# Optimization experiments

Measured on AMD Instinct MI355X. Metric: run time of the kernel, lower is better.

## Reference

```python
import jax, jax.numpy as jnp
import numpy as np
from jax import lax

T_LEN, BATCH, D_IN, D_HID, N_LAYERS = 512, 32, 512, 512, 4


def setup_inputs() -> dict:
    key = jax.random.key(0)
    kx, kw, ku = jax.random.split(key, 3)
    x = jax.random.normal(kx, (T_LEN, BATCH, D_IN), dtype=jnp.float32)
    # xavier-ish scale on input kernels to keep the relu recurrence stable
    W = jax.random.normal(kw, (N_LAYERS, D_HID, D_IN), dtype=jnp.float32) * (1.0 / np.sqrt(D_IN))
    b = jnp.zeros((N_LAYERS, D_HID), dtype=jnp.float32)
    # diagonal recurrent weights in [0,1) so |u|<=1 (non-exploding)
    u = jax.random.uniform(ku, (N_LAYERS, D_HID), dtype=jnp.float32)
    return {"x": x, "W": W, "b": b, "u": u}


def _indrnn_layer(x, W_l, b_l, u_l):
    # x: [T, B, Din]; precompute input projection as one big GEMM
    xh = jnp.einsum('tbd,hd->tbh', x, W_l) + b_l  # [T, B, Dh]
    h0 = jnp.zeros((x.shape[1], W_l.shape[0]), dtype=x.dtype)

    def step(h, xh_t):
        h_new = jax.nn.relu(xh_t + u_l * h)
        return h_new, h_new

    _, outs = lax.scan(step, h0, xh)
    return outs  # [T, B, Dh]


def reference(x, W, b, u):
    out = x
    for l in range(W.shape[0]):  # fixed small layer count
        out = _indrnn_layer(out, W[l], b[l], u[l])
    return out
```

## Files before the change

### kernel.cpp

```cpp
#include <hip/hip_runtime.h>
#include <hip/hip_bf16.h>

typedef short bf16x8 __attribute__((ext_vector_type(8)));
typedef float f32x4 __attribute__((ext_vector_type(4)));

#define T_LEN 512
#define BATCH 32
#define D 512
#define M_TOT (T_LEN * BATCH)
#define NLAYER 4

#define BM 128
#define BN 128
#define BK 64
#define NT (D / BK)
#define EP 72

#define CH 64
#define NCH (T_LEN / CH)

__global__ __launch_bounds__(256) void convert_k(const float* __restrict__ W,
                                                 const float* __restrict__ x,
                                                 __hip_bfloat16* __restrict__ Wb,
                                                 __hip_bfloat16* __restrict__ xb) {
    const int nW = NLAYER * D * D;
    const int nX = M_TOT * D;
    int i = (blockIdx.x * 256 + threadIdx.x) * 4;
    const float* src;
    __hip_bfloat16* dst;
    if (i < nW) {
        src = W + i;
        dst = Wb + i;
    } else {
        int k = i - nW;
        if (k >= nX) return;
        src = x + k;
        dst = xb + k;
    }
    float4 v = *(const float4*)src;
    __hip_bfloat16 h0 = __float2bfloat16(v.x);
    __hip_bfloat16 h1 = __float2bfloat16(v.y);
    __hip_bfloat16 h2 = __float2bfloat16(v.z);
    __hip_bfloat16 h3 = __float2bfloat16(v.w);
    ushort4 o;
    o.x = *(const unsigned short*)&h0;
    o.y = *(const unsigned short*)&h1;
    o.z = *(const unsigned short*)&h2;
    o.w = *(const unsigned short*)&h3;
    *(ushort4*)dst = o;
}

__global__ __launch_bounds__(256) void gemm_bt(const __hip_bfloat16* __restrict__ A,
                                               const __hip_bfloat16* __restrict__ Bt,
                                               const float* __restrict__ bias,
                                               __hip_bfloat16* __restrict__ Cb) {
    constexpr int K = D;
    constexpr int N = D;
    __shared__ __hip_bfloat16 smem[4 * BM * BK];
    __hip_bfloat16* const AsP[2] = {smem, smem + BM * BK};
    __hip_bfloat16* const BsP[2] = {smem + 2 * BM * BK, smem + 3 * BM * BK};

    const int tid  = threadIdx.x;
    const int wave = tid >> 6;
    const int lane = tid & 63;

    const int bid = blockIdx.x;
    const int xcd = bid & 7;
    const int j   = bid >> 3;
    const int bm  = xcd * 16 + (j >> 2);
    const int bn  = j & 3;

    const int wm = (wave >> 1) * 64;
    const int wn = (wave & 1) * 64;

    const int srow = lane >> 3;
    const int scol = ((lane & 7) ^ srow) * 8;

    const __hip_bfloat16* Ag = A  + (size_t)(bm * BM) * K;
    const __hip_bfloat16* Bg = Bt + (size_t)(bn * BN) * K;

    f32x4 acc[4][4] = {};

#define STAGE(buf, k0)                                                                               \
    do {                                                                                             \
        _Pragma("unroll") for (int jj = 0; jj < 4; ++jj) {                                           \
            const int rbase = (jj * 4 + wave) * 8;                                                   \
            __builtin_amdgcn_global_load_lds(                                                        \
                (const __attribute__((address_space(1))) void*)(Ag + (size_t)(rbase + srow) * K + (k0) + scol), \
                (__attribute__((address_space(3))) void*)(&AsP[buf][rbase * BK]), 16, 0, 0);         \
            __builtin_amdgcn_global_load_lds(                                                        \
                (const __attribute__((address_space(1))) void*)(Bg + (size_t)(rbase + srow) * K + (k0) + scol), \
                (__attribute__((address_space(3))) void*)(&BsP[buf][rbase * BK]), 16, 0, 0);         \
        }                                                                                            \
    } while (0)

#define COMPUTE(buf)                                                                                 \
    do {                                                                                             \
        bf16x8 af[4][2], bv[4][2];                                                                   \
        const int fr = lane & 15;                                                                    \
        const int kq = lane >> 4;                                                          \
        _Pragma("unroll") for (int mi = 0; mi < 4; ++mi) {                                           \
            const int r = wm + mi * 16 + fr;                                                         \
            _Pragma("unroll") for (int kh = 0; kh < 2; ++kh) {                                       \
                const int c = ((kh * 4 + kq) ^ (fr & 7)) * 8;                                        \
                af[mi][kh] = *(const bf16x8*)(&AsP[buf][r * BK + c]);                                \
            }                                                                                        \
        }                                                                                            \
        _Pragma("unroll") for (int ni = 0; ni < 4; ++ni) {                                           \
            const int r = wn + ni * 16 + fr;                                                         \
            _Pragma("unroll") for (int kh = 0; kh < 2; ++kh) {                                       \
                const int c = ((kh * 4 + kq) ^ (fr & 7)) * 8;                                        \
                bv[ni][kh] = *(const bf16x8*)(&BsP[buf][r * BK + c]);                                \
            }                                                                                        \
        }                                                                                            \
        _Pragma("unroll") for (int kh = 0; kh < 2; ++kh)                                             \
            _Pragma("unroll") for (int mi = 0; mi < 4; ++mi)                                         \
                _Pragma("unroll") for (int ni = 0; ni < 4; ++ni)                                     \
                    acc[mi][ni] = __builtin_amdgcn_mfma_f32_16x16x32_bf16(af[mi][kh], bv[ni][kh],    \
                                                                          acc[mi][ni], 0, 0, 0);    \
    } while (0)

    STAGE(0, 0);
    __syncthreads();
    int cur = 0;
#pragma unroll
    for (int kt = 1; kt < NT; ++kt) {
        STAGE(cur ^ 1, kt * BK);
        COMPUTE(cur);
        __syncthreads();
        cur ^= 1;
    }
    COMPUTE(cur);
    __syncthreads();

    {
        __hip_bfloat16* S = smem + wave * (64 * EP);
        const int cfr = lane & 15;
        const int cfq = lane >> 4;
        float bs[4];
#pragma unroll
        for (int ni = 0; ni < 4; ++ni) bs[ni] = bias[bn * BN + wn + ni * 16 + cfr];
#pragma unroll
        for (int mi = 0; mi < 4; ++mi)
#pragma unroll
            for (int ni = 0; ni < 4; ++ni)
#pragma unroll
                for (int r = 0; r < 4; ++r)
                    S[(mi * 16 + cfq * 4 + r) * EP + ni * 16 + cfr] =
                        __float2bfloat16(acc[mi][ni][r] + bs[ni]);
        const int rq = lane >> 3;
        const int cl = (lane & 7) * 8;
#pragma unroll
        for (int p = 0; p < 8; ++p) {
            const int lr = p * 8 + rq;
            bf16x8 v = *(const bf16x8*)(S + lr * EP + cl);
            *(bf16x8*)(&Cb[(size_t)(bm * BM + wm + lr) * N + bn * BN + wn + cl]) = v;
        }
    }
#undef STAGE
#undef COMPUTE
}

template <int MODE>
__global__ __launch_bounds__(512) void scan_k(const __hip_bfloat16* __restrict__ xh,
                                              const float* __restrict__ u,
                                              float* __restrict__ outf,
                                              __hip_bfloat16* __restrict__ outb) {
    __shared__ float2 md[NCH][64];
    const int i   = threadIdx.x & 63;
    const int c   = threadIdx.x >> 6;
    const int idx = blockIdx.x * 64 + i;
    const float uu = u[idx & (D - 1)];

    const __hip_bfloat16* p = xh + (size_t)c * CH * M_TOT + idx;
    unsigned short xv[CH];
#pragma unroll
    for (int t = 0; t < CH; ++t) xv[t] = *(const unsigned short*)(p + (size_t)t * M_TOT);

    float m = 0.f, d = 0.f;
#pragma unroll
    for (int t = 0; t < CH; ++t) {
        const float a = __uint_as_float(((unsigned int)xv[t]) << 16);
        m = fmaxf(fmaf(uu, m, a), 0.f);
        d = fmaf(uu, d, a);
    }
    md[c][i] = make_float2(m, d);
    __syncthreads();

    float e = uu * uu;
    e *= e; e *= e; e *= e; e *= e; e *= e;
    float h = 0.f;
    for (int jj = 0; jj < c; ++jj) {
        const float2 v = md[jj][i];
        h = fmaxf(v.x, fmaf(e, h, v.y));
    }

    float* qf = outf + (size_t)c * CH * M_TOT + idx;
    __hip_bfloat16* qb = outb + (size_t)c * CH * M_TOT + idx;
#pragma unroll
    for (int t = 0; t < CH; ++t) {
        const float a = __uint_as_float(((unsigned int)xv[t]) << 16);
        h = fmaxf(fmaf(uu, h, a), 0.f);
        if (MODE & 1) qf[(size_t)t * M_TOT] = h;
        if (MODE & 2) qb[(size_t)t * M_TOT] = __float2bfloat16(h);
    }
}

extern "C" void kernel_launch(void* const* d_in, const int* in_sizes, int n_in,
                              void* d_out, int out_size, void* d_ws, size_t ws_size,
                              hipStream_t stream) {
    const float* x = (const float*)d_in[0];
    const float* W = (const float*)d_in[1];
    const float* b = (const float*)d_in[2];
    const float* u = (const float*)d_in[3];
    float* out = (float*)d_out;

    __hip_bfloat16* Wb = (__hip_bfloat16*)d_ws;
    __hip_bfloat16* Ab = (__hip_bfloat16*)((char*)d_ws + (size_t)NLAYER * D * D * 2);
    __hip_bfloat16* Xh = Ab + (size_t)M_TOT * D;

    const int n_conv = NLAYER * D * D + M_TOT * D;
    convert_k<<<n_conv / 4 / 256, 256, 0, stream>>>(W, x, Wb, Ab);

    for (int l = 0; l < NLAYER; ++l) {
        gemm_bt<<<(M_TOT / BM) * (D / BN), 256, 0, stream>>>(Ab, Wb + (size_t)l * D * D,
                                                             b + (size_t)l * D, Xh);
        if (l < NLAYER - 1) {
            scan_k<2><<<M_TOT / 64, 512, 0, stream>>>(Xh, u + (size_t)l * D, nullptr, Ab);
        } else {
            scan_k<1><<<M_TOT / 64, 512, 0, stream>>>(Xh, u + (size_t)l * D, out, nullptr);
        }
    }
}
```

Before: 124.9 us.

## Triple-buffer larger GEMM tiles with 8 waves and pair-vectorize scan

The GEMM now uses 256x128 tiles with 512 threads and a three-slot LDS ring in dynamic shared memory, with explicit vmcnt waits, raw barriers and setprio around the MFMA block. This is meant to hide global-to-LDS latency and raise per-block reuse. The scan kernel now handles two hidden units per thread with packed 32-bit loads and stores, and uses 32-step chunks, which shortens the serial recurrence and widens memory accesses. In exchange the GEMM uses more LDS and registers, launches fewer blocks (which can hurt occupancy), and relies on hand-managed synchronization.

```diff
diff --git a/kernel.cpp b/kernel.cpp
--- a/kernel.cpp
+++ b/kernel.cpp
@@ -10,14 +10,32 @@
 #define M_TOT (T_LEN * BATCH)
 #define NLAYER 4
 
-#define BM 128
+#define BM 256
 #define BN 128
 #define BK 64
 #define NT (D / BK)
+#define TILE_ELEMS (BM * BK + BN * BK)
+#define SMEM_BYTES (3 * TILE_ELEMS * 2)
 #define EP 72
 
-#define CH 64
+#define CH 32
 #define NCH (T_LEN / CH)
+
+#define SBAR()                                  \
+    do {                                        \
+        __builtin_amdgcn_s_barrier();           \
+        __builtin_amdgcn_sched_barrier(0);      \
+    } while (0)
+#define VMCNT6()                                             \
+    do {                                                     \
+        asm volatile("s_waitcnt vmcnt(6)" ::: "memory");     \
+        __builtin_amdgcn_sched_barrier(0);                   \
+    } while (0)
+#define VMCNT0()                                             \
+    do {                                                     \
+        asm volatile("s_waitcnt vmcnt(0)" ::: "memory");     \
+        __builtin_amdgcn_sched_barrier(0);                   \
+    } while (0)
 
 __global__ __launch_bounds__(256) void convert_k(const float* __restrict__ W,
                                                  const float* __restrict__ x,
@@ -50,15 +68,13 @@
     *(ushort4*)dst = o;
 }
 
-__global__ __launch_bounds__(256) void gemm_bt(const __hip_bfloat16* __restrict__ A,
-                                               const __hip_bfloat16* __restrict__ Bt,
-                                               const float* __restrict__ bias,
-                                               __hip_bfloat16* __restrict__ Cb) {
+__global__ __launch_bounds__(512, 2) void gemm_bt(const __hip_bfloat16* __restrict__ A,
+                                                  const __hip_bfloat16* __restrict__ Bt,
+                                                  const float* __restrict__ bias,
+                                                  __hip_bfloat16* __restrict__ Cb) {
     constexpr int K = D;
     constexpr int N = D;
-    __shared__ __hip_bfloat16 smem[4 * BM * BK];
-    __hip_bfloat16* const AsP[2] = {smem, smem + BM * BK};
-    __hip_bfloat16* const BsP[2] = {smem + 2 * BM * BK, smem + 3 * BM * BK};
+    extern __shared__ __hip_bfloat16 smem[];
 
     const int tid  = threadIdx.x;
     const int wave = tid >> 6;
@@ -67,11 +83,11 @@
     const int bid = blockIdx.x;
     const int xcd = bid & 7;
     const int j   = bid >> 3;
-    const int bm  = xcd * 16 + (j >> 2);
+    const int bm  = xcd * 8 + (j >> 2);
     const int bn  = j & 3;
 
-    const int wm = (wave >> 1) * 64;
-    const int wn = (wave & 1) * 64;
+    const int wm3 = wave >> 1;
+    const int wn1 = wave & 1;
 
     const int srow = lane >> 3;
     const int scol = ((lane & 7) ^ srow) * 8;
@@ -81,57 +97,74 @@
 
     f32x4 acc[4][4] = {};
 
-#define STAGE(buf, k0)                                                                               \
+#define STAGE(slot, k0)                                                                              \
     do {                                                                                             \
+        __hip_bfloat16* const Asl = smem + (slot) * TILE_ELEMS;                                      \
+        __hip_bfloat16* const Bsl = Asl + BM * BK;                                                   \
         _Pragma("unroll") for (int jj = 0; jj < 4; ++jj) {                                           \
-            const int rbase = (jj * 4 + wave) * 8;                                                   \
+            const int rbase = (wave * 4 + jj) * 8;                                                   \
             __builtin_amdgcn_global_load_lds(                                                        \
                 (const __attribute__((address_space(1))) void*)(Ag + (size_t)(rbase + srow) * K + (k0) + scol), \
-                (__attribute__((address_space(3))) void*)(&AsP[buf][rbase * BK]), 16, 0, 0);         \
+                (__attribute__((address_space(3))) void*)(Asl + rbase * BK), 16, 0, 0);              \
+        }                                                                                            \
+        _Pragma("unroll") for (int jj = 0; jj < 2; ++jj) {                                           \
+            const int rbase = (wave * 2 + jj) * 8;                                                   \
             __builtin_amdgcn_global_load_lds(                                                        \
                 (const __attribute__((address_space(1))) void*)(Bg + (size_t)(rbase + srow) * K + (k0) + scol), \
-                (__attribute__((address_space(3))) void*)(&BsP[buf][rbase * BK]), 16, 0, 0);         \
-        }                                                                                            \
-    } while (0)
-
-#define COMPUTE(buf)                                                                                 \
+                (__attribute__((address_space(3))) void*)(Bsl + rbase * BK), 16, 0, 0);              \
+        }                                                                                            \
+    } while (0)
+
+#define COMPUTE(slot)                                                                                \
     do {                                                                                             \
+        const __hip_bfloat16* const Asl = smem + (slot) * TILE_ELEMS;                                \
+        const __hip_bfloat16* const Bsl = Asl + BM * BK;                                             \
         bf16x8 af[4][2], bv[4][2];                                                                   \
         const int fr = lane & 15;                                                                    \
-        const int kq = lane >> 4;                                                          \
+        const int kq = lane >> 4;                                                                    \
         _Pragma("unroll") for (int mi = 0; mi < 4; ++mi) {                                           \
-            const int r = wm + mi * 16 + fr;                                                         \
+            const int r = wm3 * 64 + mi * 16 + fr;                                                   \
             _Pragma("unroll") for (int kh = 0; kh < 2; ++kh) {                                       \
                 const int c = ((kh * 4 + kq) ^ (fr & 7)) * 8;                                        \
-                af[mi][kh] = *(const bf16x8*)(&AsP[buf][r * BK + c]);                                \
+                af[mi][kh] = *(const bf16x8*)(&Asl[r * BK + c]);                                     \
             }                                                                                        \
         }                                                                                            \
         _Pragma("unroll") for (int ni = 0; ni < 4; ++ni) {                                           \
-            const int r = wn + ni * 16 + fr;                                                         \
+            const int r = wn1 * 64 + ni * 16 + fr;                                                   \
             _Pragma("unroll") for (int kh = 0; kh < 2; ++kh) {                                       \
                 const int c = ((kh * 4 + kq) ^ (fr & 7)) * 8;                                        \
-                bv[ni][kh] = *(const bf16x8*)(&BsP[buf][r * BK + c]);                                \
+                bv[ni][kh] = *(const bf16x8*)(&Bsl[r * BK + c]);                                     \
             }                                                                                        \
         }                                                                                            \
+        __builtin_amdgcn_s_setprio(1);                                                               \
         _Pragma("unroll") for (int kh = 0; kh < 2; ++kh)                                             \
             _Pragma("unroll") for (int mi = 0; mi < 4; ++mi)                                         \
                 _Pragma("unroll") for (int ni = 0; ni < 4; ++ni)                                     \
                     acc[mi][ni] = __builtin_amdgcn_mfma_f32_16x16x32_bf16(af[mi][kh], bv[ni][kh],    \
                                                                           acc[mi][ni], 0, 0, 0);    \
+        __builtin_amdgcn_s_setprio(0);                                                               \
     } while (0)
 
     STAGE(0, 0);
-    __syncthreads();
-    int cur = 0;
-#pragma unroll
-    for (int kt = 1; kt < NT; ++kt) {
-        STAGE(cur ^ 1, kt * BK);
-        COMPUTE(cur);
-        __syncthreads();
-        cur ^= 1;
-    }
-    COMPUTE(cur);
-    __syncthreads();
+    STAGE(1, BK);
+    VMCNT6();
+    SBAR();
+
+#pragma unroll
+    for (int t = 0; t < NT; ++t) {
+        COMPUTE(t % 3);
+        if (t < NT - 1) {
+            SBAR();
+            if (t + 2 < NT) STAGE((t + 2) % 3, (t + 2) * BK);
+            if (t < NT - 2) {
+                VMCNT6();
+            } else {
+                VMCNT0();
+            }
+            SBAR();
+        }
+    }
+    SBAR();
 
     {
         __hip_bfloat16* S = smem + wave * (64 * EP);
@@ -139,7 +172,7 @@
         const int cfq = lane >> 4;
         float bs[4];
 #pragma unroll
-        for (int ni = 0; ni < 4; ++ni) bs[ni] = bias[bn * BN + wn + ni * 16 + cfr];
+        for (int ni = 0; ni < 4; ++ni) bs[ni] = bias[bn * BN + wn1 * 64 + ni * 16 + cfr];
 #pragma unroll
         for (int mi = 0; mi < 4; ++mi)
 #pragma unroll
@@ -154,7 +187,7 @@
         for (int p = 0; p < 8; ++p) {
             const int lr = p * 8 + rq;
             bf16x8 v = *(const bf16x8*)(S + lr * EP + cl);
-            *(bf16x8*)(&Cb[(size_t)(bm * BM + wm + lr) * N + bn * BN + wn + cl]) = v;
+            *(bf16x8*)(&Cb[(size_t)(bm * BM + wm3 * 64 + lr) * N + bn * BN + wn1 * 64 + cl]) = v;
         }
     }
 #undef STAGE
@@ -166,43 +199,57 @@
                                               const float* __restrict__ u,
                                               float* __restrict__ outf,
                                               __hip_bfloat16* __restrict__ outb) {
-    __shared__ float2 md[NCH][64];
-    const int i   = threadIdx.x & 63;
-    const int c   = threadIdx.x >> 6;
-    const int idx = blockIdx.x * 64 + i;
-    const float uu = u[idx & (D - 1)];
+    __shared__ float4 md[NCH][32];
+    const int i2  = threadIdx.x & 31;
+    const int c   = threadIdx.x >> 5;
+    const int idx = blockIdx.x * 64 + i2 * 2;
+    const float u0 = u[idx & (D - 1)];
+    const float u1 = u[(idx + 1) & (D - 1)];
 
     const __hip_bfloat16* p = xh + (size_t)c * CH * M_TOT + idx;
-    unsigned short xv[CH];
-#pragma unroll
-    for (int t = 0; t < CH; ++t) xv[t] = *(const unsigned short*)(p + (size_t)t * M_TOT);
-
-    float m = 0.f, d = 0.f;
+    unsigned int xv[CH];
+#pragma unroll
+    for (int t = 0; t < CH; ++t) xv[t] = *(const unsigned int*)(p + (size_t)t * M_TOT);
+
+    float m0 = 0.f, d0 = 0.f, m1 = 0.f, d1 = 0.f;
 #pragma unroll
     for (int t = 0; t < CH; ++t) {
-        const float a = __uint_as_float(((unsigned int)xv[t]) << 16);
-        m = fmaxf(fmaf(uu, m, a), 0.f);
-        d = fmaf(uu, d, a);
-    }
-    md[c][i] = make_float2(m, d);
+        const float a0 = __uint_as_float(xv[t] << 16);
+        const float a1 = __uint_as_float(xv[t] & 0xffff0000u);
+        m0 = fmaxf(fmaf(u0, m0, a0), 0.f);
+        d0 = fmaf(u0, d0, a0);
+        m1 = fmaxf(fmaf(u1, m1, a1), 0.f);
+        d1 = fmaf(u1, d1, a1);
+    }
+    md[c][i2] = make_float4(m0, d0, m1, d1);
     __syncthreads();
 
-    float e = uu * uu;
-    e *= e; e *= e; e *= e; e *= e; e *= e;
-    float h = 0.f;
+    float e0 = u0 * u0, e1 = u1 * u1;
+    e0 *= e0; e0 *= e0; e0 *= e0; e0 *= e0;
+    e1 *= e1; e1 *= e1; e1 *= e1; e1 *= e1;
+    float h0 = 0.f, h1 = 0.f;
     for (int jj = 0; jj < c; ++jj) {
-        const float2 v = md[jj][i];
-        h = fmaxf(v.x, fmaf(e, h, v.y));
-    }
-
-    float* qf = outf + (size_t)c * CH * M_TOT + idx;
-    __hip_bfloat16* qb = outb + (size_t)c * CH * M_TOT + idx;
+        const float4 v = md[jj][i2];
+        h0 = fmaxf(v.x, fmaf(e0, h0, v.y));
+        h1 = fmaxf(v.z, fmaf(e1, h1, v.w));
+    }
+
+    const size_t base = (size_t)c * CH * M_TOT + idx;
 #pragma unroll
     for (int t = 0; t < CH; ++t) {
-        const float a = __uint_as_float(((unsigned int)xv[t]) << 16);
-        h = fmaxf(fmaf(uu, h, a), 0.f);
-        if (MODE & 1) qf[(size_t)t * M_TOT] = h;
-        if (MODE & 2) qb[(size_t)t * M_TOT] = __float2bfloat16(h);
+        const size_t off = base + (size_t)t * M_TOT;
+        const float a0 = __uint_as_float(xv[t] << 16);
+        const float a1 = __uint_as_float(xv[t] & 0xffff0000u);
+        h0 = fmaxf(fmaf(u0, h0, a0), 0.f);
+        h1 = fmaxf(fmaf(u1, h1, a1), 0.f);
+        if (MODE & 1) *(float2*)(outf + off) = make_float2(h0, h1);
+        if (MODE & 2) {
+            __hip_bfloat16 b0 = __float2bfloat16(h0);
+            __hip_bfloat16 b1 = __float2bfloat16(h1);
+            unsigned int pk = (unsigned int)(*(unsigned short*)&b0) |
+                              ((unsigned int)(*(unsigned short*)&b1) << 16);
+            *(unsigned int*)(outb + off) = pk;
+        }
     }
 }
 
@@ -219,12 +266,15 @@
     __hip_bfloat16* Ab = (__hip_bfloat16*)((char*)d_ws + (size_t)NLAYER * D * D * 2);
     __hip_bfloat16* Xh = Ab + (size_t)M_TOT * D;
 
+    (void)hipFuncSetAttribute((const void*)gemm_bt,
+                              hipFuncAttributeMaxDynamicSharedMemorySize, SMEM_BYTES);
+
     const int n_conv = NLAYER * D * D + M_TOT * D;
     convert_k<<<n_conv / 4 / 256, 256, 0, stream>>>(W, x, Wb, Ab);
 
     for (int l = 0; l < NLAYER; ++l) {
-        gemm_bt<<<(M_TOT / BM) * (D / BN), 256, 0, stream>>>(Ab, Wb + (size_t)l * D * D,
-                                                             b + (size_t)l * D, Xh);
+        gemm_bt<<<(M_TOT / BM) * (D / BN), 512, SMEM_BYTES, stream>>>(
+            Ab, Wb + (size_t)l * D * D, b + (size_t)l * D, Xh);
         if (l < NLAYER - 1) {
             scan_k<2><<<M_TOT / 64, 512, 0, stream>>>(Xh, u + (size_t)l * D, nullptr, Ab);
         } else {
```

Result: slower. 129.8 us (+3.9%).
